# Performance work log

Measured on AMD Instinct MI355X. Metric: run time of the kernel, lower is better.

## Reference

```python
import jax, jax.numpy as jnp
import numpy as np

B, D, H, E, O = 524288, 32, 64, 8, 1
H2 = H // 2


def setup_inputs() -> dict:
    key = jax.random.key(0)
    ks = jax.random.split(key, 6)
    x = jax.random.normal(ks[0], (B, D), dtype=jnp.float32)
    soft_cluster_probs = jax.random.uniform(ks[1], (B, E), dtype=jnp.float32)
    # Stacked per-expert MLP params (Dense default glorot-like scale approximated by scaled normal)
    W1 = jax.random.normal(ks[2], (E, D, H), dtype=jnp.float32) * (1.0 / np.sqrt(D))
    b1 = jnp.zeros((E, H), dtype=jnp.float32)
    W2 = jax.random.normal(ks[3], (E, H, H2), dtype=jnp.float32) * (1.0 / np.sqrt(H))
    b2 = jnp.zeros((E, H2), dtype=jnp.float32)
    W3 = jax.random.normal(ks[4], (E, H2, O), dtype=jnp.float32) * (1.0 / np.sqrt(H2))
    b3 = jnp.zeros((E, O), dtype=jnp.float32)
    return {"x": x, "soft_cluster_probs": soft_cluster_probs,
            "W1": W1, "b1": b1, "W2": W2, "b2": b2, "W3": W3, "b3": b3}


def reference(x, soft_cluster_probs, W1, b1, W2, b2, W3, b3):
    # Soft-clustering inference path: every expert processes all rows,
    # outputs combined with per-row expert weights. Dropout inactive.
    h1 = jax.nn.relu(jnp.einsum('bd,edh->ebh', x, W1) + b1[:, None, :])      # [E,B,H]
    h2 = jax.nn.relu(jnp.einsum('ebh,ehk->ebk', h1, W2) + b2[:, None, :])    # [E,B,H/2]
    eo = jax.nn.sigmoid(jnp.einsum('ebk,eko->ebo', h2, W3) + b3[:, None, :])  # [E,B,O]
    # combined = sum_e eo[e] * clustering[:, e:e+1]
    out = jnp.einsum('ebo,be->bo', eo, soft_cluster_probs)                    # [B,O]
    return out
```

## Files before the change

### kernel.cpp

```cpp
#include <hip/hip_runtime.h>


typedef __attribute__((ext_vector_type(8))) _Float16 f16x8;
typedef __attribute__((ext_vector_type(2))) __fp16 h16x2;
typedef __attribute__((ext_vector_type(4))) float f32x4;

__device__ __forceinline__ unsigned pkh(float lo, float hi) {
    union { h16x2 v; unsigned u; } t;
    t.v = __builtin_amdgcn_cvt_pkrtz(lo, hi);
    return t.u;
}

__device__ __forceinline__ unsigned relu2(unsigned a) {
    unsigned r;
    asm("v_pk_max_f16 %0, %1, 0" : "=v"(r) : "v"(a));
    return r;
}

#define MFMA32(a, b, c) __builtin_amdgcn_mfma_f32_16x16x32_f16((a), (b), (c), 0, 0, 0)

__global__ __launch_bounds__(1024)
void build_image(const float* __restrict__ W1, const float* __restrict__ b1,
                 const float* __restrict__ W2, const float* __restrict__ b2,
                 const float* __restrict__ W3, const float* __restrict__ b3,
                 char* __restrict__ ws) {
    const int tid = threadIdx.x;
    #pragma unroll
    for (int k = 0; k < 4; ++k) {
        const int F = tid + k * 1024;
        const int e = (F >> 8) & 7, s = F & 255;
        const int qq = (s >> 4) & 3, nn = s & 15;
        const float* src;
        int stride;
        if (F < 2048) {
            const int mt = s >> 6;
            const int h = 32 * (mt >> 1) + 8 * (nn >> 2) + 4 * (mt & 1) + (nn & 3);
            src = W1 + (e * 32 + 8 * qq) * 64 + h;
            stride = 64;
        } else {
            const int kb2 = (s >> 7) & 1, mt2 = (s >> 6) & 1;
            const int h2 = 8 * (nn >> 2) + 4 * mt2 + (nn & 3);
            src = W2 + (e * 64 + 32 * kb2 + 8 * qq) * 32 + h2;
            stride = 32;
        }
        union { f16x8 v; unsigned u[4]; } t;
        t.u[0] = pkh(src[0 * stride], src[1 * stride]);
        t.u[1] = pkh(src[2 * stride], src[3 * stride]);
        t.u[2] = pkh(src[4 * stride], src[5 * stride]);
        t.u[3] = pkh(src[6 * stride], src[7 * stride]);
        *(f16x8*)(ws + F * 16) = t.v;
    }
    if (tid < 128) {
        const int e = tid >> 4, mt = (tid >> 2) & 3, q = tid & 3;
        *(f32x4*)(ws + 65536 + tid * 16) =
            *(const f32x4*)(b1 + e * 64 + 32 * (mt >> 1) + 4 * (mt & 1) + 8 * q);
    } else if (tid < 192) {
        const int i = tid - 128, e = i >> 3, mt2 = (i >> 2) & 1, q = i & 3;
        *(f32x4*)(ws + 67584 + i * 16) =
            *(const f32x4*)(b2 + e * 32 + 4 * mt2 + 8 * q);
    } else if (tid < 224) {
        const int i = tid - 192, e = i >> 2, q = i & 3;
        const f32x4 lo = *(const f32x4*)(W3 + e * 32 + 8 * q);
        const f32x4 hi = *(const f32x4*)(W3 + e * 32 + 8 * q + 4);
        union { f16x8 v; unsigned u[4]; } a;
        a.u[0] = pkh(lo.x, lo.y); a.u[1] = pkh(lo.z, lo.w);
        a.u[2] = pkh(hi.x, hi.y); a.u[3] = pkh(hi.z, hi.w);
        *(f16x8*)(ws + 68608 + i * 16) = a.v;
    } else if (tid < 232) {
        const int i = tid - 224;
        *(float*)(ws + 69120 + i * 4) = b3[i];
    }
}

__global__ __launch_bounds__(1024, 8)
void moe_fused(const float* __restrict__ x, const float* __restrict__ probs,
               const char* __restrict__ img, float* __restrict__ out) {
    __shared__ __attribute__((aligned(16))) char ldsraw[69632];
    const int tid = threadIdx.x;
    const int w = tid >> 6, lane = tid & 63, n = lane & 15, q = lane >> 4;

    #pragma unroll
    for (int k = 0; k < 4; ++k) {
        const int off = tid * 16 + k * 16384;
        *(f32x4*)(ldsraw + off) = *(const f32x4*)(img + off);
    }
    if (tid < 226) {
        const int off = 65536 + tid * 16;
        *(f32x4*)(ldsraw + off) = *(const f32x4*)(img + off);
    }

    const int rb = blockIdx.x * 512 + w * 32;
    const float* xp0 = x + (size_t)(rb + n) * 32 + q * 8;
    const float* xp1 = xp0 + 16 * 32;
    const f32x4 xa0 = *(const f32x4*)xp0, xb0 = *(const f32x4*)(xp0 + 4);
    const f32x4 xa1 = *(const f32x4*)xp1, xb1 = *(const f32x4*)(xp1 + 4);
    union { f16x8 v; unsigned u[4]; } xf0, xf1;
    xf0.u[0] = pkh(xa0.x, xa0.y); xf0.u[1] = pkh(xa0.z, xa0.w);
    xf0.u[2] = pkh(xb0.x, xb0.y); xf0.u[3] = pkh(xb0.z, xb0.w);
    xf1.u[0] = pkh(xa1.x, xa1.y); xf1.u[1] = pkh(xa1.z, xa1.w);
    xf1.u[2] = pkh(xb1.x, xb1.y); xf1.u[3] = pkh(xb1.z, xb1.w);

    __syncthreads();

    const short* wl = (const short*)ldsraw + (n * 8 + q * 128);
    const char* bb1 = ldsraw + 65536 + q * 16;
    const char* bb2 = ldsraw + 67584 + q * 16;
    const char* ba3 = ldsraw + 68608 + q * 16;
    const float* pba = probs + (size_t)(rb + n) * 8;
    float r0 = 0.f, r1 = 0.f;

    #pragma unroll 4
    for (int e = 0; e < 8; ++e) {
        const float pb0 = pba[e], pb1 = pba[e + 128];
        const short* we = wl + e * 2048;

        union { f16x8 v; unsigned u[4]; } P0[2], P1[2];
        #pragma unroll
        for (int mt = 0; mt < 4; ++mt) {
            const f16x8 w1f = *(const f16x8*)(we + mt * 512);
            const f32x4 bf = *(const f32x4*)(bb1 + e * 256 + mt * 64);
            const f32x4 c0 = MFMA32(w1f, xf0.v, bf);
            const f32x4 c1 = MFMA32(w1f, xf1.v, bf);
            P0[mt >> 1].u[(mt & 1) * 2 + 0] = relu2(pkh(c0.x, c0.y));
            P0[mt >> 1].u[(mt & 1) * 2 + 1] = relu2(pkh(c0.z, c0.w));
            P1[mt >> 1].u[(mt & 1) * 2 + 0] = relu2(pkh(c1.x, c1.y));
            P1[mt >> 1].u[(mt & 1) * 2 + 1] = relu2(pkh(c1.z, c1.w));
        }

        union { f16x8 v; unsigned u[4]; } PC0, PC1;
        #pragma unroll
        for (int mt2 = 0; mt2 < 2; ++mt2) {
            const f32x4 bf = *(const f32x4*)(bb2 + e * 128 + mt2 * 64);
            f32x4 c0 = bf, c1 = bf;
            #pragma unroll
            for (int kb2 = 0; kb2 < 2; ++kb2) {
                const f16x8 w2f =
                    *(const f16x8*)(we + 16384 + mt2 * 512 + kb2 * 1024);
                c0 = MFMA32(w2f, P0[kb2].v, c0);
                c1 = MFMA32(w2f, P1[kb2].v, c1);
            }
            PC0.u[mt2 * 2 + 0] = relu2(pkh(c0.x, c0.y));
            PC0.u[mt2 * 2 + 1] = relu2(pkh(c0.z, c0.w));
            PC1.u[mt2 * 2 + 0] = relu2(pkh(c1.x, c1.y));
            PC1.u[mt2 * 2 + 1] = relu2(pkh(c1.z, c1.w));
        }

        const f16x8 a3v = *(const f16x8*)(ba3 + e * 64);
        const float bb = *(const float*)(ldsraw + 69120 + e * 4);
        const f32x4 cb = {bb, bb, bb, bb};
        const f32x4 s0 = MFMA32(a3v, PC0.v, cb);
        const f32x4 s1 = MFMA32(a3v, PC1.v, cb);

        r0 = fmaf(1.f / (1.f + __expf(-s0.x)), pb0, r0);
        r1 = fmaf(1.f / (1.f + __expf(-s1.x)), pb1, r1);
    }

    if (q == 0) {
        out[rb + n] = r0;
        out[rb + 16 + n] = r1;
    }
}

extern "C" void kernel_launch(void* const* d_in, const int* in_sizes, int n_in,
                              void* d_out, int out_size, void* d_ws, size_t ws_size,
                              hipStream_t stream) {
    const float* x     = (const float*)d_in[0];
    const float* probs = (const float*)d_in[1];
    const float* W1    = (const float*)d_in[2];
    const float* b1    = (const float*)d_in[3];
    const float* W2    = (const float*)d_in[4];
    const float* b2    = (const float*)d_in[5];
    const float* W3    = (const float*)d_in[6];
    const float* b3    = (const float*)d_in[7];

    hipLaunchKernelGGL(build_image, dim3(1), dim3(1024), 0, stream,
                       W1, b1, W2, b2, W3, b3, (char*)d_ws);
    const int nrows = in_sizes[0] / 32;
    hipLaunchKernelGGL(moe_fused, dim3(nrows / 512), dim3(1024), 0, stream,
                       x, probs, (const char*)d_ws, (float*)d_out);
}
```

Before: 145.1 us.

## Process four row tiles per wave with 512-thread blocks and global-loaded biases

```diff
diff --git a/kernel.cpp b/kernel.cpp
--- a/kernel.cpp
+++ b/kernel.cpp
@@ -15,6 +15,10 @@
     unsigned r;
     asm("v_pk_max_f16 %0, %1, 0" : "=v"(r) : "v"(a));
     return r;
+}
+
+__device__ __forceinline__ float sigf(float s) {
+    return 1.f / (1.f + __expf(-s));
 }
 
 #define MFMA32(a, b, c) __builtin_amdgcn_mfma_f32_16x16x32_f16((a), (b), (c), 0, 0, 0)
@@ -72,92 +76,93 @@
     }
 }
 
-__global__ __launch_bounds__(1024, 8)
+__global__ __launch_bounds__(512, 4)
 void moe_fused(const float* __restrict__ x, const float* __restrict__ probs,
                const char* __restrict__ img, float* __restrict__ out) {
-    __shared__ __attribute__((aligned(16))) char ldsraw[69632];
+    __shared__ __attribute__((aligned(16))) char ldsraw[65536];
     const int tid = threadIdx.x;
     const int w = tid >> 6, lane = tid & 63, n = lane & 15, q = lane >> 4;
 
     #pragma unroll
-    for (int k = 0; k < 4; ++k) {
-        const int off = tid * 16 + k * 16384;
-        *(f32x4*)(ldsraw + off) = *(const f32x4*)(img + off);
-    }
-    if (tid < 226) {
-        const int off = 65536 + tid * 16;
+    for (int k = 0; k < 8; ++k) {
+        const int off = tid * 16 + k * 8192;
         *(f32x4*)(ldsraw + off) = *(const f32x4*)(img + off);
     }
 
-    const int rb = blockIdx.x * 512 + w * 32;
-    const float* xp0 = x + (size_t)(rb + n) * 32 + q * 8;
-    const float* xp1 = xp0 + 16 * 32;
-    const f32x4 xa0 = *(const f32x4*)xp0, xb0 = *(const f32x4*)(xp0 + 4);
-    const f32x4 xa1 = *(const f32x4*)xp1, xb1 = *(const f32x4*)(xp1 + 4);
-    union { f16x8 v; unsigned u[4]; } xf0, xf1;
-    xf0.u[0] = pkh(xa0.x, xa0.y); xf0.u[1] = pkh(xa0.z, xa0.w);
-    xf0.u[2] = pkh(xb0.x, xb0.y); xf0.u[3] = pkh(xb0.z, xb0.w);
-    xf1.u[0] = pkh(xa1.x, xa1.y); xf1.u[1] = pkh(xa1.z, xa1.w);
-    xf1.u[2] = pkh(xb1.x, xb1.y); xf1.u[3] = pkh(xb1.z, xb1.w);
+    const int rb = blockIdx.x * 512 + w * 64;
+    union { f16x8 v; unsigned u[4]; } xf[4];
+    #pragma unroll
+    for (int rt = 0; rt < 4; ++rt) {
+        const float* xp = x + (size_t)(rb + rt * 16 + n) * 32 + q * 8;
+        const f32x4 xa = *(const f32x4*)xp, xb = *(const f32x4*)(xp + 4);
+        xf[rt].u[0] = pkh(xa.x, xa.y); xf[rt].u[1] = pkh(xa.z, xa.w);
+        xf[rt].u[2] = pkh(xb.x, xb.y); xf[rt].u[3] = pkh(xb.z, xb.w);
+    }
 
     __syncthreads();
 
     const short* wl = (const short*)ldsraw + (n * 8 + q * 128);
-    const char* bb1 = ldsraw + 65536 + q * 16;
-    const char* bb2 = ldsraw + 67584 + q * 16;
-    const char* ba3 = ldsraw + 68608 + q * 16;
+    const char* gb1 = img + 65536 + q * 16;
+    const char* gb2 = img + 67584 + q * 16;
+    const char* ga3 = img + 68608 + q * 16;
+    const float* gb3 = (const float*)(img + 69120);
     const float* pba = probs + (size_t)(rb + n) * 8;
-    float r0 = 0.f, r1 = 0.f;
+    float r[4] = {0.f, 0.f, 0.f, 0.f};
 
-    #pragma unroll 4
+    #pragma unroll 1
     for (int e = 0; e < 8; ++e) {
-        const float pb0 = pba[e], pb1 = pba[e + 128];
         const short* we = wl + e * 2048;
 
-        union { f16x8 v; unsigned u[4]; } P0[2], P1[2];
+        union { f16x8 v; unsigned u[4]; } P[4][2];
         #pragma unroll
         for (int mt = 0; mt < 4; ++mt) {
             const f16x8 w1f = *(const f16x8*)(we + mt * 512);
-            const f32x4 bf = *(const f32x4*)(bb1 + e * 256 + mt * 64);
-            const f32x4 c0 = MFMA32(w1f, xf0.v, bf);
-            const f32x4 c1 = MFMA32(w1f, xf1.v, bf);
-            P0[mt >> 1].u[(mt & 1) * 2 + 0] = relu2(pkh(c0.x, c0.y));
-            P0[mt >> 1].u[(mt & 1) * 2 + 1] = relu2(pkh(c0.z, c0.w));
-            P1[mt >> 1].u[(mt & 1) * 2 + 0] = relu2(pkh(c1.x, c1.y));
-            P1[mt >> 1].u[(mt & 1) * 2 + 1] = relu2(pkh(c1.z, c1.w));
+            const f32x4 bf = *(const f32x4*)(gb1 + e * 256 + mt * 64);
+            f32x4 c[4];
+            #pragma unroll
+            for (int rt = 0; rt < 4; ++rt) c[rt] = MFMA32(w1f, xf[rt].v, bf);
+            #pragma unroll
+            for (int rt = 0; rt < 4; ++rt) {
+                P[rt][mt >> 1].u[(mt & 1) * 2 + 0] = relu2(pkh(c[rt].x, c[rt].y));
+                P[rt][mt >> 1].u[(mt & 1) * 2 + 1] = relu2(pkh(c[rt].z, c[rt].w));
+            }
         }
 
-        union { f16x8 v; unsigned u[4]; } PC0, PC1;
+        union { f16x8 v; unsigned u[4]; } PC[4];
         #pragma unroll
         for (int mt2 = 0; mt2 < 2; ++mt2) {
-            const f32x4 bf = *(const f32x4*)(bb2 + e * 128 + mt2 * 64);
-            f32x4 c0 = bf, c1 = bf;
+            const f32x4 bf = *(const f32x4*)(gb2 + e * 128 + mt2 * 64);
+            f32x4 c[4];
+            #pragma unroll
+            for (int rt = 0; rt < 4; ++rt) c[rt] = bf;
             #pragma unroll
             for (int kb2 = 0; kb2 < 2; ++kb2) {
                 const f16x8 w2f =
                     *(const f16x8*)(we + 16384 + mt2 * 512 + kb2 * 1024);
-                c0 = MFMA32(w2f, P0[kb2].v, c0);
-                c1 = MFMA32(w2f, P1[kb2].v, c1);
+                #pragma unroll
+                for (int rt = 0; rt < 4; ++rt)
+                    c[rt] = MFMA32(w2f, P[rt][kb2].v, c[rt]);
             }
-            PC0.u[mt2 * 2 + 0] = relu2(pkh(c0.x, c0.y));
-            PC0.u[mt2 * 2 + 1] = relu2(pkh(c0.z, c0.w));
-            PC1.u[mt2 * 2 + 0] = relu2(pkh(c1.x, c1.y));
-            PC1.u[mt2 * 2 + 1] = relu2(pkh(c1.z, c1.w));
+            #pragma unroll
+            for (int rt = 0; rt < 4; ++rt) {
+                PC[rt].u[mt2 * 2 + 0] = relu2(pkh(c[rt].x, c[rt].y));
+                PC[rt].u[mt2 * 2 + 1] = relu2(pkh(c[rt].z, c[rt].w));
+            }
         }
 
-        const f16x8 a3v = *(const f16x8*)(ba3 + e * 64);
-        const float bb = *(const float*)(ldsraw + 69120 + e * 4);
+        const f16x8 a3v = *(const f16x8*)(ga3 + e * 64);
+        const float bb = gb3[e];
         const f32x4 cb = {bb, bb, bb, bb};
-        const f32x4 s0 = MFMA32(a3v, PC0.v, cb);
-        const f32x4 s1 = MFMA32(a3v, PC1.v, cb);
-
-        r0 = fmaf(1.f / (1.f + __expf(-s0.x)), pb0, r0);
-        r1 = fmaf(1.f / (1.f + __expf(-s1.x)), pb1, r1);
+        #pragma unroll
+        for (int rt = 0; rt < 4; ++rt) {
+            const f32x4 s = MFMA32(a3v, PC[rt].v, cb);
+            r[rt] = fmaf(sigf(s.x), pba[e + rt * 128], r[rt]);
+        }
     }
 
     if (q == 0) {
-        out[rb + n] = r0;
-        out[rb + 16 + n] = r1;
+        #pragma unroll
+        for (int rt = 0; rt < 4; ++rt) out[rb + rt * 16 + n] = r[rt];
     }
 }
 
@@ -176,6 +181,6 @@
     hipLaunchKernelGGL(build_image, dim3(1), dim3(1024), 0, stream,
                        W1, b1, W2, b2, W3, b3, (char*)d_ws);
     const int nrows = in_sizes[0] / 32;
-    hipLaunchKernelGGL(moe_fused, dim3(nrows / 512), dim3(1024), 0, stream,
+    hipLaunchKernelGGL(moe_fused, dim3(nrows / 512), dim3(512), 0, stream,
                        x, probs, (const char*)d_ws, (float*)d_out);
 }
```

Result: slower. 156.2 us (+7.7%).
